# Optimization experiments

Measured on AMD Instinct MI355X. Metric: run time of the kernel, lower is better.

Reference implementation:

```python
import jax, jax.numpy as jnp
import numpy as np

B, INPUT_DIM, N = 8, 1, 4096
DIM, DEPTH, HEADS, DIM_HEAD = 512, 4, 8, 64
WINDOW = 128
NUM_CLASSES = 10
INNER = int(DIM * 4 * 2 / 3)  # 1365 (GEGLU FeedForward inner dim)
LN_EPS = 1e-5


def setup_inputs() -> dict:
    key = jax.random.key(0)
    ks = jax.random.split(key, 12)
    s = 0.02
    inner_qkv = HEADS * DIM_HEAD
    return {
        "x": jax.random.normal(ks[0], (B, INPUT_DIM, N), dtype=jnp.float32),
        "lin_emb_w": jax.random.normal(ks[1], (DIM, INPUT_DIM), dtype=jnp.float32) * s,
        "lin_emb_b": jnp.zeros((DIM,), dtype=jnp.float32),
        "qkv_w": jax.random.normal(ks[2], (DEPTH, 3 * inner_qkv, DIM), dtype=jnp.float32) * s,
        "out_w": jax.random.normal(ks[3], (DEPTH, DIM, inner_qkv), dtype=jnp.float32) * s,
        "ff_ln_g": jnp.ones((DEPTH, DIM), dtype=jnp.float32),
        "ff_ln_b": jnp.zeros((DEPTH, DIM), dtype=jnp.float32),
        "ff_w1": jax.random.normal(ks[4], (DEPTH, 2 * INNER, DIM), dtype=jnp.float32) * s,
        "ff_w2": jax.random.normal(ks[5], (DEPTH, DIM, INNER), dtype=jnp.float32) * s,
        "proj_w": jax.random.normal(ks[6], (NUM_CLASSES, DIM), dtype=jnp.float32) * s,
        "proj_b": jnp.zeros((NUM_CLASSES,), dtype=jnp.float32),
    }


def _layer_norm(x, g, b):
    mu = jnp.mean(x, axis=-1, keepdims=True)
    var = jnp.mean(jnp.square(x - mu), axis=-1, keepdims=True)
    return (x - mu) * jax.lax.rsqrt(var + LN_EPS) * g + b


def _local_attention(q, k, v, w):
    # q,k,v: (b, h, n, d). Non-causal sliding window: each window of size w
    # attends to windows [i-1, i, i+1] (look_backward=1, look_forward=1),
    # with out-of-range key positions masked (lucidrains LocalAttention,
    # autopad=True, exact_windowsize=False). n is a multiple of w here.
    b, h, n, d = q.shape
    nw = n // w
    scale = d ** -0.5
    qw = q.reshape(b, h, nw, w, d) * scale
    kw = k.reshape(b, h, nw, w, d)
    vw = v.reshape(b, h, nw, w, d)

    def look_around(t):  # (b,h,nw,w,d) -> (b,h,nw,3w,d)
        tp = jnp.pad(t, ((0, 0), (0, 0), (1, 1), (0, 0), (0, 0)))
        return jnp.concatenate([tp[:, :, i:i + nw] for i in range(3)], axis=3)

    k3 = look_around(kw)
    v3 = look_around(vw)

    # validity mask for boundary windows (fake keys from padding)
    win = jnp.arange(nw)
    kpos = (win[:, None] - 1) * w + jnp.arange(3 * w)[None, :]  # (nw, 3w)
    valid = (kpos >= 0) & (kpos < n)

    scores = jnp.einsum('bhnqd,bhnkd->bhnqk', qw, k3)  # (b,h,nw,w,3w)
    scores = jnp.where(valid[None, None, :, None, :], scores,
                       jnp.finfo(scores.dtype).min)
    attn = jax.nn.softmax(scores, axis=-1)
    out = jnp.einsum('bhnqk,bhnkd->bhnqd', attn, v3)
    return out.reshape(b, h, n, d)


def reference(x, lin_emb_w, lin_emb_b, qkv_w, out_w, ff_ln_g, ff_ln_b,
              ff_w1, ff_w2, proj_w, proj_b):
    b = x.shape[0]
    h = jnp.einsum('bdn,ed->bne', x, lin_emb_w) + lin_emb_b  # (b, n, dim)
    for l in range(DEPTH):
        # --- LocalMHA (no prenorm) + residual ---
        qkv = jnp.einsum('bnd,ed->bne', h, qkv_w[l])
        q, k, v = jnp.split(qkv, 3, axis=-1)
        def heads(t):
            return t.reshape(b, N, HEADS, DIM_HEAD).transpose(0, 2, 1, 3)
        o = _local_attention(heads(q), heads(k), heads(v), WINDOW)
        o = o.transpose(0, 2, 1, 3).reshape(b, N, HEADS * DIM_HEAD)
        h = jnp.einsum('bne,de->bnd', o, out_w[l]) + h
        # --- GEGLU FeedForward (prenorm inside) + residual ---
        y = _layer_norm(h, ff_ln_g[l], ff_ln_b[l])
        y = jnp.einsum('bnd,ed->bne', y, ff_w1[l])
        u, gate = jnp.split(y, 2, axis=-1)
        y = u * jax.nn.gelu(gate, approximate=False)
        h = h + jnp.einsum('bne,de->bnd', y, ff_w2[l])
    pooled = h.mean(axis=1)  # mean_pooling
    return pooled @ proj_w.T + proj_b
```

## Files before the change

### kernel.cpp

```cpp
#include <hip/hip_runtime.h>
#include <hip/hip_bf16.h>
#include <math.h>

typedef __attribute__((ext_vector_type(8))) short short8;
typedef __attribute__((ext_vector_type(4))) float f32x4;

__device__ __forceinline__ short f2bf(float f){
  unsigned u = __float_as_uint(f);
  u = (u + 0x7FFFu + ((u >> 16) & 1u)) >> 16;
  return (short)u;
}

__global__ void cast_bf16_kernel(const float* __restrict__ s, short* __restrict__ d, int n){
  int i = blockIdx.x * 256 + threadIdx.x;
  if (i < n) d[i] = f2bf(s[i]);
}

__global__ void w1p_kernel(const float* __restrict__ s, short* __restrict__ d){
  int i = blockIdx.x * 256 + threadIdx.x;
  int c  = i & 511;
  int rl = i >> 9;
  int r  = rl % 2816;
  int l  = rl / 2816;
  float v = 0.f;
  if (r < 2730){
    int sr = (r & 1) ? (1365 + (r >> 1)) : (r >> 1);
    v = s[((size_t)l * 2730 + sr) * 512 + c];
  }
  d[i] = f2bf(v);
}

__global__ void w2p_kernel(const float* __restrict__ s, short* __restrict__ d){
  int i = blockIdx.x * 256 + threadIdx.x;
  int c = i % 1408;
  int r = i / 1408;
  float v = (c < 1365) ? s[(size_t)r * 1365 + c] : 0.f;
  d[i] = f2bf(v);
}

__global__ void embed_kernel(const float* __restrict__ x, const float* __restrict__ w,
                             const float* __restrict__ bias, float* __restrict__ hf,
                             short* __restrict__ hb){
  long i = (long)blockIdx.x * 256 + threadIdx.x;
  long row = i >> 9; int e = (int)(i & 511);
  float v = x[row] * w[e] + bias[e];
  hf[i] = v;
  hb[i] = f2bf(v);
}

template<int EPI>
__global__ __launch_bounds__(256, 2)
void gemm_bt(const short* __restrict__ A, const short* __restrict__ B, int K,
             float* __restrict__ Cres, short* __restrict__ Cbf, int ldcb)
{
  __shared__ short As[128 * 64];
  __shared__ short Bs[128 * 64];
  const int tid  = threadIdx.x;
  const int lane = tid & 63;
  const int w    = tid >> 6;
  const int wr   = (w >> 1) * 64, wc = (w & 1) * 64;
  const long tm = (long)blockIdx.y * 128, tn = (long)blockIdx.x * 128;

  f32x4 acc[4][4];
  #pragma unroll
  for (int i = 0; i < 4; i++)
    #pragma unroll
    for (int j = 0; j < 4; j++)
      acc[i][j] = (f32x4){0.f, 0.f, 0.f, 0.f};

  const int row_s = tid >> 3;
  const int c_s   = tid & 7;

  for (int k0 = 0; k0 < K; k0 += 64){
    __syncthreads();
    #pragma unroll
    for (int r = 0; r < 4; r++){
      int row = row_s + r * 32;
      short8 av = *(const short8*)(A + (tm + row) * K + k0 + c_s * 8);
      short8 bv = *(const short8*)(B + (tn + row) * K + k0 + c_s * 8);
      int off = (row * 128 + c_s * 16) ^ ((row & 7) << 4);
      *(short8*)((char*)As + off) = av;
      *(short8*)((char*)Bs + off) = bv;
    }
    __syncthreads();
    #pragma unroll
    for (int kk = 0; kk < 2; kk++){
      short8 a[4], b[4];
      int ac = (kk * 32 + (lane >> 4) * 8) * 2;
      #pragma unroll
      for (int i = 0; i < 4; i++){
        int ar = wr + i * 16 + (lane & 15);
        a[i] = *(const short8*)((char*)As + ((ar * 128 + ac) ^ ((ar & 7) << 4)));
        int br = wc + i * 16 + (lane & 15);
        b[i] = *(const short8*)((char*)Bs + ((br * 128 + ac) ^ ((br & 7) << 4)));
      }
      #pragma unroll
      for (int i = 0; i < 4; i++)
        #pragma unroll
        for (int j = 0; j < 4; j++)
          acc[i][j] = __builtin_amdgcn_mfma_f32_16x16x32_bf16(a[i], b[j], acc[i][j], 0, 0, 0);
    }
  }

  #pragma unroll
  for (int i = 0; i < 4; i++){
    #pragma unroll
    for (int j = 0; j < 4; j++){
      #pragma unroll
      for (int v = 0; v < 4; v++){
        long row = tm + wr + i * 16 + (lane >> 4) * 4 + v;
        long col = tn + wc + j * 16 + (lane & 15);
        float x = acc[i][j][v];
        if (EPI == 0){
          Cbf[row * ldcb + col] = f2bf(x);
        } else if (EPI == 1){
          float rr = x + Cres[row * 512 + col];
          Cres[row * 512 + col] = rr;
        } else if (EPI == 2){
          float rr = x + Cres[row * 512 + col];
          Cres[row * 512 + col] = rr;
          Cbf[row * 512 + col] = f2bf(rr);
        } else {
          float other = __shfl_xor(x, 1);
          if ((lane & 1) == 0){
            float gate = other;
            float gg = 0.5f * gate * (1.f + erff(gate * 0.70710678118f));
            Cbf[row * ldcb + (col >> 1)] = f2bf(x * gg);
          }
        }
      }
    }
  }
}

__global__ __launch_bounds__(256, 2)
void attn_kernel(const short* __restrict__ qkv, short* __restrict__ o)
{
  __shared__ short Ks[128 * 64];
  __shared__ short Vt[64 * 136];
  __shared__ short Ps[4 * 32 * 128];
  const int win = blockIdx.x, hh = blockIdx.y, b = blockIdx.z;
  const int tid = threadIdx.x, lane = tid & 63, w = tid >> 6;
  const long qrow0 = (long)b * 4096 + (long)win * 128;

  short8 qf[2][2];
  #pragma unroll
  for (int i = 0; i < 2; i++)
    #pragma unroll
    for (int kk = 0; kk < 2; kk++)
      qf[i][kk] = *(const short8*)(qkv + (qrow0 + w * 32 + i * 16 + (lane & 15)) * 1536
                                   + hh * 64 + kk * 32 + (lane >> 4) * 8);

  f32x4 oacc[2][4];
  #pragma unroll
  for (int i = 0; i < 2; i++)
    #pragma unroll
    for (int j = 0; j < 4; j++)
      oacc[i][j] = (f32x4){0.f, 0.f, 0.f, 0.f};
  float rs[2][4];
  #pragma unroll
  for (int i = 0; i < 2; i++)
    #pragma unroll
    for (int v = 0; v < 4; v++)
      rs[i][v] = 0.f;

  const int row_s = tid >> 3, c_s = tid & 7;
  for (int cc = 0; cc < 3; cc++){
    int kw = win - 1 + cc;
    if (kw < 0 || kw >= 32) continue;
    const long krow0 = (long)b * 4096 + (long)kw * 128;
    __syncthreads();
    #pragma unroll
    for (int r = 0; r < 4; r++){
      int row = row_s + r * 32;
      const short* src = qkv + (krow0 + row) * 1536 + hh * 64;
      short8 kv = *(const short8*)(src + 512 + c_s * 8);
      *(short8*)((char*)Ks + ((row * 128 + c_s * 16) ^ ((row & 7) << 4))) = kv;
      short8 vv = *(const short8*)(src + 1024 + c_s * 8);
      #pragma unroll
      for (int e = 0; e < 8; e++) Vt[(c_s * 8 + e) * 136 + row] = vv[e];
    }
    __syncthreads();

    f32x4 sacc[2][8];
    #pragma unroll
    for (int i = 0; i < 2; i++)
      #pragma unroll
      for (int j = 0; j < 8; j++)
        sacc[i][j] = (f32x4){0.f, 0.f, 0.f, 0.f};
    #pragma unroll
    for (int kk = 0; kk < 2; kk++){
      short8 bb[8];
      int ac = (kk * 32 + (lane >> 4) * 8) * 2;
      #pragma unroll
      for (int j = 0; j < 8; j++){
        int br = j * 16 + (lane & 15);
        bb[j] = *(const short8*)((char*)Ks + ((br * 128 + ac) ^ ((br & 7) << 4)));
      }
      #pragma unroll
      for (int i = 0; i < 2; i++)
        #pragma unroll
        for (int j = 0; j < 8; j++)
          sacc[i][j] = __builtin_amdgcn_mfma_f32_16x16x32_bf16(qf[i][kk], bb[j], sacc[i][j], 0, 0, 0);
    }

    short* myPs = Ps + w * 32 * 128;
    float psum[2][4];
    #pragma unroll
    for (int i = 0; i < 2; i++)
      #pragma unroll
      for (int v = 0; v < 4; v++)
        psum[i][v] = 0.f;
    #pragma unroll
    for (int i = 0; i < 2; i++)
      #pragma unroll
      for (int j = 0; j < 8; j++)
        #pragma unroll
        for (int v = 0; v < 4; v++){
          float p = expf(0.125f * sacc[i][j][v]);
          psum[i][v] += p;
          int prow = i * 16 + (lane >> 4) * 4 + v;
          int pcb  = (j * 16 + (lane & 15)) * 2;
          *(short*)((char*)myPs + ((prow * 256 + pcb) ^ ((prow & 7) << 4))) = f2bf(p);
        }
    #pragma unroll
    for (int i = 0; i < 2; i++)
      #pragma unroll
      for (int v = 0; v < 4; v++){
        float s = psum[i][v];
        s += __shfl_xor(s, 1); s += __shfl_xor(s, 2);
        s += __shfl_xor(s, 4); s += __shfl_xor(s, 8);
        rs[i][v] += s;
      }
    __syncthreads();

    #pragma unroll
    for (int kk = 0; kk < 4; kk++){
      short8 pa[2], vb[4];
      int kb = (kk * 32 + (lane >> 4) * 8) * 2;
      #pragma unroll
      for (int i = 0; i < 2; i++){
        int pr = i * 16 + (lane & 15);
        pa[i] = *(const short8*)((char*)myPs + ((pr * 256 + kb) ^ ((pr & 7) << 4)));
      }
      #pragma unroll
      for (int j = 0; j < 4; j++){
        int vr = j * 16 + (lane & 15);
        vb[j] = *(const short8*)((char*)Vt + (vr * 272 + kb));
      }
      #pragma unroll
      for (int i = 0; i < 2; i++)
        #pragma unroll
        for (int j = 0; j < 4; j++)
          oacc[i][j] = __builtin_amdgcn_mfma_f32_16x16x32_bf16(pa[i], vb[j], oacc[i][j], 0, 0, 0);
    }
  }

  #pragma unroll
  for (int i = 0; i < 2; i++)
    #pragma unroll
    for (int j = 0; j < 4; j++)
      #pragma unroll
      for (int v = 0; v < 4; v++){
        long row = qrow0 + w * 32 + i * 16 + (lane >> 4) * 4 + v;
        int col = hh * 64 + j * 16 + (lane & 15);
        o[row * 512 + col] = f2bf(oacc[i][j][v] / rs[i][v]);
      }
}

__global__ __launch_bounds__(256)
void ln_kernel(const float* __restrict__ h, const float* __restrict__ g,
               const float* __restrict__ be, short* __restrict__ y)
{
  long row = (long)blockIdx.x * 4 + (threadIdx.x >> 6);
  int lane = threadIdx.x & 63;
  const float* x = h + row * 512 + lane * 8;
  float4 a0 = *(const float4*)x;
  float4 a1 = *(const float4*)(x + 4);
  float v[8] = {a0.x, a0.y, a0.z, a0.w, a1.x, a1.y, a1.z, a1.w};
  float s = 0.f, sq = 0.f;
  #pragma unroll
  for (int j = 0; j < 8; j++){ s += v[j]; sq += v[j] * v[j]; }
  #pragma unroll
  for (int m = 1; m <= 32; m <<= 1){ s += __shfl_xor(s, m); sq += __shfl_xor(sq, m); }
  float mu = s * (1.f / 512.f);
  float var = sq * (1.f / 512.f) - mu * mu;
  float rstd = rsqrtf(var + 1e-5f);
  short* yo = y + row * 512 + lane * 8;
  #pragma unroll
  for (int j = 0; j < 8; j++){
    int c = lane * 8 + j;
    yo[j] = f2bf((v[j] - mu) * rstd * g[c] + be[c]);
  }
}

__global__ void pool_partial(const float* __restrict__ h, float* __restrict__ part){
  int b = blockIdx.x, ch = blockIdx.y, t = threadIdx.x;
  float s0 = 0.f, s1 = 0.f;
  const float* base = h + ((long)b * 4096 + ch * 128) * 512;
  for (int n = 0; n < 128; n++){
    s0 += base[(long)n * 512 + t];
    s1 += base[(long)n * 512 + t + 256];
  }
  part[((b * 32 + ch) * 512) + t] = s0;
  part[((b * 32 + ch) * 512) + t + 256] = s1;
}

__global__ void pool_proj(const float* __restrict__ part, const float* __restrict__ pw,
                          const float* __restrict__ pb, float* __restrict__ out){
  __shared__ float pooled[512];
  __shared__ float red[4];
  int b = blockIdx.x, t = threadIdx.x;
  int lane = t & 63, w = t >> 6;
  float s0 = 0.f, s1 = 0.f;
  for (int ch = 0; ch < 32; ch++){
    s0 += part[((b * 32 + ch) * 512) + t];
    s1 += part[((b * 32 + ch) * 512) + t + 256];
  }
  pooled[t] = s0 * (1.f / 4096.f);
  pooled[t + 256] = s1 * (1.f / 4096.f);
  __syncthreads();
  for (int cls = 0; cls < 10; cls++){
    float p = pooled[t] * pw[cls * 512 + t] + pooled[t + 256] * pw[cls * 512 + t + 256];
    p += __shfl_xor(p, 1); p += __shfl_xor(p, 2); p += __shfl_xor(p, 4);
    p += __shfl_xor(p, 8); p += __shfl_xor(p, 16); p += __shfl_xor(p, 32);
    if (lane == 0) red[w] = p;
    __syncthreads();
    if (t == 0) out[b * 10 + cls] = red[0] + red[1] + red[2] + red[3] + pb[cls];
    __syncthreads();
  }
}

extern "C" void kernel_launch(void* const* d_in, const int* in_sizes, int n_in,
                              void* d_out, int out_size, void* d_ws, size_t ws_size,
                              hipStream_t stream)
{
  const float* x      = (const float*)d_in[0];
  const float* lin_w  = (const float*)d_in[1];
  const float* lin_b  = (const float*)d_in[2];
  const float* qkvw_f = (const float*)d_in[3];
  const float* outw_f = (const float*)d_in[4];
  const float* lng    = (const float*)d_in[5];
  const float* lnb    = (const float*)d_in[6];
  const float* w1_f   = (const float*)d_in[7];
  const float* w2_f   = (const float*)d_in[8];
  const float* projw  = (const float*)d_in[9];
  const float* projb  = (const float*)d_in[10];
  float* out = (float*)d_out;

  char* ws = (char*)d_ws;
  float* hf32 = (float*)(ws);
  short* abuf = (short*)(ws + 67108864);
  short* qkvb = (short*)(ws + 100663296);
  short* gbuf = qkvb;
  short* obuf = (short*)(ws + 201326592);
  float* part = (float*)(ws + 234881024);
  short* wqkv = (short*)(ws + 235405312);
  short* wout = (short*)(ws + 247988224);
  short* w1p  = (short*)(ws + 250085376);
  short* w2p  = (short*)(ws + 261619712);

  cast_bf16_kernel<<<12288, 256, 0, stream>>>(qkvw_f, wqkv, 4 * 1536 * 512);
  cast_bf16_kernel<<<4096, 256, 0, stream>>>(outw_f, wout, 4 * 512 * 512);
  w1p_kernel<<<22528, 256, 0, stream>>>(w1_f, w1p);
  w2p_kernel<<<11264, 256, 0, stream>>>(w2_f, w2p);
  embed_kernel<<<65536, 256, 0, stream>>>(x, lin_w, lin_b, hf32, abuf);

  for (int l = 0; l < 4; l++){
    gemm_bt<0><<<dim3(12, 256), 256, 0, stream>>>(abuf, wqkv + (size_t)l * 1536 * 512, 512,
                                                  nullptr, qkvb, 1536);
    attn_kernel<<<dim3(32, 8, 8), 256, 0, stream>>>(qkvb, obuf);
    gemm_bt<1><<<dim3(4, 256), 256, 0, stream>>>(obuf, wout + (size_t)l * 512 * 512, 512,
                                                 hf32, nullptr, 0);
    ln_kernel<<<8192, 256, 0, stream>>>(hf32, lng + l * 512, lnb + l * 512, abuf);
    gemm_bt<3><<<dim3(22, 256), 256, 0, stream>>>(abuf, w1p + (size_t)l * 2816 * 512, 512,
                                                  nullptr, gbuf, 1408);
    gemm_bt<2><<<dim3(4, 256), 256, 0, stream>>>(gbuf, w2p + (size_t)l * 512 * 1408, 1408,
                                                 hf32, abuf, 512);
  }
  pool_partial<<<dim3(8, 32), 256, 0, stream>>>(hf32, part);
  pool_proj<<<8, 256, 0, stream>>>(part, projw, projb, out);
}
```

Measured before the change: 1.916 ms.

## Replace 128x128 GEMM with pipelined 256x256 direct-to-LDS double-buffered GEMM

Replaces the 128x128 tiled GEMM with a 256x256-tile, 512-thread kernel. It uses global_load_lds direct copies into a double-buffered shared memory ring, interleaves prefetch with MFMA phases under explicit barriers and setprio, and adds XCD-aware block swizzling. The GEGLU weight layout is regrouped in blocks of 16 so u and gate land in adjacent accumulator tiles, which removes the cross-lane shuffle. erff is replaced by a polynomial approximation. The risks are tail quantization with fewer, larger tiles, a heavy LDS footprint of 128KB that limits occupancy, and the approximation error of the polynomial GELU.

```diff
diff --git a/kernel.cpp b/kernel.cpp
--- a/kernel.cpp
+++ b/kernel.cpp
@@ -4,11 +4,22 @@
 
 typedef __attribute__((ext_vector_type(8))) short short8;
 typedef __attribute__((ext_vector_type(4))) float f32x4;
+
+#define MFMA16 __builtin_amdgcn_mfma_f32_16x16x32_bf16
 
 __device__ __forceinline__ short f2bf(float f){
   unsigned u = __float_as_uint(f);
   u = (u + 0x7FFFu + ((u >> 16) & 1u)) >> 16;
   return (short)u;
+}
+
+__device__ __forceinline__ float gelu_phi(float g){
+  float ax = fabsf(g) * 0.70710678118f;
+  float t  = 1.f / (1.f + 0.3275911f * ax);
+  float pp = ((((1.061405429f * t - 1.453152027f) * t + 1.421413741f) * t
+               - 0.284496736f) * t + 0.254829592f) * t;
+  float e  = 1.f - pp * __expf(-ax * ax);
+  return 0.5f + copysignf(0.5f, g) * e;
 }
 
 __global__ void cast_bf16_kernel(const float* __restrict__ s, short* __restrict__ d, int n){
@@ -22,9 +33,11 @@
   int rl = i >> 9;
   int r  = rl % 2816;
   int l  = rl / 2816;
+  int g  = r >> 5, sfx = r & 31;
+  int j  = g * 16 + (sfx & 15);
   float v = 0.f;
-  if (r < 2730){
-    int sr = (r & 1) ? (1365 + (r >> 1)) : (r >> 1);
+  if (j < 1365){
+    int sr = (sfx < 16) ? j : 1365 + j;
     v = s[((size_t)l * 2730 + sr) * 512 + c];
   }
   d[i] = f2bf(v);
@@ -49,83 +62,171 @@
 }
 
 template<int EPI>
-__global__ __launch_bounds__(256, 2)
-void gemm_bt(const short* __restrict__ A, const short* __restrict__ B, int K,
+__global__ __launch_bounds__(512, 2)
+void gemm256(const short* __restrict__ A, const short* __restrict__ B, int K,
              float* __restrict__ Cres, short* __restrict__ Cbf, int ldcb)
 {
-  __shared__ short As[128 * 64];
-  __shared__ short Bs[128 * 64];
+  __shared__ short As[2][256][64];
+  __shared__ short Bs[2][256][64];
+  char* smA = (char*)As;
+  char* smB = (char*)Bs;
+
   const int tid  = threadIdx.x;
   const int lane = tid & 63;
   const int w    = tid >> 6;
-  const int wr   = (w >> 1) * 64, wc = (w & 1) * 64;
-  const long tm = (long)blockIdx.y * 128, tn = (long)blockIdx.x * 128;
-
-  f32x4 acc[4][4];
-  #pragma unroll
-  for (int i = 0; i < 4; i++)
+  const int wm   = w >> 2;
+  const int wn   = w & 3;
+  const int NT   = K >> 6;
+
+  const int nwg = gridDim.x * gridDim.y;
+  const int f   = blockIdx.y * gridDim.x + blockIdx.x;
+  const int sw  = (f & 7) * (nwg >> 3) + (f >> 3);
+  const long tm = (long)(sw / gridDim.x) * 256;
+  const long tn = (long)(sw % gridDim.x) * 256;
+
+  const int r0 = tid >> 3;
+  const int c0 = (tid & 7) ^ (r0 & 7);
+  const short* aS = A + (tm + r0) * (long)K + c0 * 8;
+  const short* bS = B + (tn + r0) * (long)K + c0 * 8;
+  const int ldsW0 = w * 1024;
+  const int ldsW1 = 8192 + w * 1024;
+  const long halfA = 128 * (long)K;
+
+  auto stgA = [&](int dstoff, const short* srcp){
+    __builtin_amdgcn_global_load_lds((const __attribute__((address_space(1))) void*)(srcp),
+        (__attribute__((address_space(3))) void*)(smA + dstoff + ldsW0), 16, 0, 0);
+    __builtin_amdgcn_global_load_lds((const __attribute__((address_space(1))) void*)(srcp + 64 * (long)K),
+        (__attribute__((address_space(3))) void*)(smA + dstoff + ldsW1), 16, 0, 0);
+  };
+  auto stgB = [&](int dstoff, const short* srcp){
+    __builtin_amdgcn_global_load_lds((const __attribute__((address_space(1))) void*)(srcp),
+        (__attribute__((address_space(3))) void*)(smB + dstoff + ldsW0), 16, 0, 0);
+    __builtin_amdgcn_global_load_lds((const __attribute__((address_space(1))) void*)(srcp + 64 * (long)K),
+        (__attribute__((address_space(3))) void*)(smB + dstoff + ldsW1), 16, 0, 0);
+  };
+
+  f32x4 acc[8][4];
+  #pragma unroll
+  for (int i = 0; i < 8; i++)
     #pragma unroll
     for (int j = 0; j < 4; j++)
       acc[i][j] = (f32x4){0.f, 0.f, 0.f, 0.f};
 
-  const int row_s = tid >> 3;
-  const int c_s   = tid & 7;
-
-  for (int k0 = 0; k0 < K; k0 += 64){
-    __syncthreads();
-    #pragma unroll
-    for (int r = 0; r < 4; r++){
-      int row = row_s + r * 32;
-      short8 av = *(const short8*)(A + (tm + row) * K + k0 + c_s * 8);
-      short8 bv = *(const short8*)(B + (tn + row) * K + k0 + c_s * 8);
-      int off = (row * 128 + c_s * 16) ^ ((row & 7) << 4);
-      *(short8*)((char*)As + off) = av;
-      *(short8*)((char*)Bs + off) = bv;
-    }
-    __syncthreads();
-    #pragma unroll
-    for (int kk = 0; kk < 2; kk++){
-      short8 a[4], b[4];
-      int ac = (kk * 32 + (lane >> 4) * 8) * 2;
-      #pragma unroll
-      for (int i = 0; i < 4; i++){
-        int ar = wr + i * 16 + (lane & 15);
-        a[i] = *(const short8*)((char*)As + ((ar * 128 + ac) ^ ((ar & 7) << 4)));
-        int br = wc + i * 16 + (lane & 15);
-        b[i] = *(const short8*)((char*)Bs + ((br * 128 + ac) ^ ((br & 7) << 4)));
-      }
-      #pragma unroll
-      for (int i = 0; i < 4; i++)
+  const int rb  = (lane & 15) * 128;
+  const int ct0 = (((lane >> 4)    ) ^ (lane & 7)) * 16;
+  const int ct1 = ((4 + (lane >> 4)) ^ (lane & 7)) * 16;
+
+  stgB(0,             bS);
+  stgA(0,             aS);
+  stgA(16384,         aS + halfA);
+  stgB(16384,         bS + halfA);
+  if (NT > 1){
+    stgB(32768,         bS + 64);
+    stgA(32768,         aS + 64);
+    stgA(32768 + 16384, aS + halfA + 64);
+  }
+  asm volatile("s_waitcnt vmcnt(6)" ::: "memory");
+  __builtin_amdgcn_s_barrier();
+
+  for (int t = 0; t < NT; ++t){
+    const int cur = (t & 1) * 32768;
+    const int nxt = 32768 - cur;
+    const bool s1 = (t + 1 < NT), s2 = (t + 2 < NT);
+    const long o1 = (long)(t + 1) * 64, o2 = (long)(t + 2) * 64;
+    short8 a0[8], a1[8], bb[4][2];
+
+    #pragma unroll
+    for (int ni = 0; ni < 4; ni++){
+      bb[ni][0] = *(const short8*)(smB + cur + wn * 8192 + ni * 2048 + rb + ct0);
+      bb[ni][1] = *(const short8*)(smB + cur + wn * 8192 + ni * 2048 + rb + ct1);
+    }
+    #pragma unroll
+    for (int mi = 0; mi < 8; mi++)
+      a0[mi] = *(const short8*)(smA + cur + wm * 16384 + mi * 2048 + rb + ct0);
+    if (s1) stgB(nxt + 16384, bS + halfA + o1);
+    asm volatile("s_waitcnt lgkmcnt(0)" ::: "memory");
+    __builtin_amdgcn_sched_barrier(0);
+    __builtin_amdgcn_s_barrier();
+    __builtin_amdgcn_s_setprio(1);
+    #pragma unroll
+    for (int mi = 0; mi < 8; mi++){
+      acc[mi][0] = MFMA16(a0[mi], bb[0][0], acc[mi][0], 0, 0, 0);
+      acc[mi][1] = MFMA16(a0[mi], bb[1][0], acc[mi][1], 0, 0, 0);
+    }
+    __builtin_amdgcn_s_setprio(0);
+    __builtin_amdgcn_s_barrier();
+
+    #pragma unroll
+    for (int mi = 0; mi < 8; mi++)
+      a1[mi] = *(const short8*)(smA + cur + wm * 16384 + mi * 2048 + rb + ct1);
+    if (s2) stgB(cur, bS + o2);
+    asm volatile("s_waitcnt lgkmcnt(0)" ::: "memory");
+    __builtin_amdgcn_sched_barrier(0);
+    __builtin_amdgcn_s_barrier();
+    __builtin_amdgcn_s_setprio(1);
+    #pragma unroll
+    for (int mi = 0; mi < 8; mi++){
+      acc[mi][2] = MFMA16(a0[mi], bb[2][0], acc[mi][2], 0, 0, 0);
+      acc[mi][3] = MFMA16(a0[mi], bb[3][0], acc[mi][3], 0, 0, 0);
+    }
+    __builtin_amdgcn_s_setprio(0);
+    __builtin_amdgcn_s_barrier();
+
+    if (s2) stgA(cur, aS + o2);
+    __builtin_amdgcn_s_barrier();
+    __builtin_amdgcn_s_setprio(1);
+    #pragma unroll
+    for (int mi = 0; mi < 8; mi++){
+      acc[mi][0] = MFMA16(a1[mi], bb[0][1], acc[mi][0], 0, 0, 0);
+      acc[mi][1] = MFMA16(a1[mi], bb[1][1], acc[mi][1], 0, 0, 0);
+    }
+    __builtin_amdgcn_s_setprio(0);
+    __builtin_amdgcn_s_barrier();
+
+    if (s2) stgA(cur + 16384, aS + halfA + o2);
+    if (t < NT - 2) asm volatile("s_waitcnt vmcnt(6)" ::: "memory");
+    else            asm volatile("s_waitcnt vmcnt(0)" ::: "memory");
+    __builtin_amdgcn_s_barrier();
+    __builtin_amdgcn_s_setprio(1);
+    #pragma unroll
+    for (int mi = 0; mi < 8; mi++){
+      acc[mi][2] = MFMA16(a1[mi], bb[2][1], acc[mi][2], 0, 0, 0);
+      acc[mi][3] = MFMA16(a1[mi], bb[3][1], acc[mi][3], 0, 0, 0);
+    }
+    __builtin_amdgcn_s_setprio(0);
+    __builtin_amdgcn_s_barrier();
+  }
+
+  #pragma unroll
+  for (int mi = 0; mi < 8; mi++){
+    if (EPI == 3){
+      #pragma unroll
+      for (int p = 0; p < 2; p++){
         #pragma unroll
-        for (int j = 0; j < 4; j++)
-          acc[i][j] = __builtin_amdgcn_mfma_f32_16x16x32_bf16(a[i], b[j], acc[i][j], 0, 0, 0);
-    }
-  }
-
-  #pragma unroll
-  for (int i = 0; i < 4; i++){
-    #pragma unroll
-    for (int j = 0; j < 4; j++){
-      #pragma unroll
-      for (int v = 0; v < 4; v++){
-        long row = tm + wr + i * 16 + (lane >> 4) * 4 + v;
-        long col = tn + wc + j * 16 + (lane & 15);
-        float x = acc[i][j][v];
-        if (EPI == 0){
-          Cbf[row * ldcb + col] = f2bf(x);
-        } else if (EPI == 1){
-          float rr = x + Cres[row * 512 + col];
-          Cres[row * 512 + col] = rr;
-        } else if (EPI == 2){
-          float rr = x + Cres[row * 512 + col];
-          Cres[row * 512 + col] = rr;
-          Cbf[row * 512 + col] = f2bf(rr);
-        } else {
-          float other = __shfl_xor(x, 1);
-          if ((lane & 1) == 0){
-            float gate = other;
-            float gg = 0.5f * gate * (1.f + erff(gate * 0.70710678118f));
-            Cbf[row * ldcb + (col >> 1)] = f2bf(x * gg);
+        for (int v = 0; v < 4; v++){
+          long row = tm + wm * 128 + mi * 16 + (lane >> 4) * 4 + v;
+          long col = (tn >> 1) + wn * 32 + p * 16 + (lane & 15);
+          float u = acc[mi][2 * p][v];
+          float g = acc[mi][2 * p + 1][v];
+          Cbf[row * ldcb + col] = f2bf(u * g * gelu_phi(g));
+        }
+      }
+    } else {
+      #pragma unroll
+      for (int ni = 0; ni < 4; ni++){
+        #pragma unroll
+        for (int v = 0; v < 4; v++){
+          long row = tm + wm * 128 + mi * 16 + (lane >> 4) * 4 + v;
+          long col = tn + wn * 64 + ni * 16 + (lane & 15);
+          float x = acc[mi][ni][v];
+          if (EPI == 0){
+            Cbf[row * ldcb + col] = f2bf(x);
+          } else if (EPI == 1){
+            Cres[row * 512 + col] = x + Cres[row * 512 + col];
+          } else {
+            float rr = x + Cres[row * 512 + col];
+            Cres[row * 512 + col] = rr;
+            Cbf[row * 512 + col] = f2bf(rr);
           }
         }
       }
@@ -190,18 +291,18 @@
         sacc[i][j] = (f32x4){0.f, 0.f, 0.f, 0.f};
     #pragma unroll
     for (int kk = 0; kk < 2; kk++){
-      short8 bb[8];
+      short8 bbk[8];
       int ac = (kk * 32 + (lane >> 4) * 8) * 2;
       #pragma unroll
       for (int j = 0; j < 8; j++){
         int br = j * 16 + (lane & 15);
-        bb[j] = *(const short8*)((char*)Ks + ((br * 128 + ac) ^ ((br & 7) << 4)));
+        bbk[j] = *(const short8*)((char*)Ks + ((br * 128 + ac) ^ ((br & 7) << 4)));
       }
       #pragma unroll
       for (int i = 0; i < 2; i++)
         #pragma unroll
         for (int j = 0; j < 8; j++)
-          sacc[i][j] = __builtin_amdgcn_mfma_f32_16x16x32_bf16(qf[i][kk], bb[j], sacc[i][j], 0, 0, 0);
+          sacc[i][j] = MFMA16(qf[i][kk], bbk[j], sacc[i][j], 0, 0, 0);
     }
 
     short* myPs = Ps + w * 32 * 128;
@@ -252,7 +353,7 @@
       for (int i = 0; i < 2; i++)
         #pragma unroll
         for (int j = 0; j < 4; j++)
-          oacc[i][j] = __builtin_amdgcn_mfma_f32_16x16x32_bf16(pa[i], vb[j], oacc[i][j], 0, 0, 0);
+          oacc[i][j] = MFMA16(pa[i], vb[j], oacc[i][j], 0, 0, 0);
     }
   }
 
@@ -367,15 +468,15 @@
   embed_kernel<<<65536, 256, 0, stream>>>(x, lin_w, lin_b, hf32, abuf);
 
   for (int l = 0; l < 4; l++){
-    gemm_bt<0><<<dim3(12, 256), 256, 0, stream>>>(abuf, wqkv + (size_t)l * 1536 * 512, 512,
-                                                  nullptr, qkvb, 1536);
+    gemm256<0><<<dim3(6, 128), 512, 0, stream>>>(abuf, wqkv + (size_t)l * 1536 * 512, 512,
+                                                 nullptr, qkvb, 1536);
     attn_kernel<<<dim3(32, 8, 8), 256, 0, stream>>>(qkvb, obuf);
-    gemm_bt<1><<<dim3(4, 256), 256, 0, stream>>>(obuf, wout + (size_t)l * 512 * 512, 512,
+    gemm256<1><<<dim3(2, 128), 512, 0, stream>>>(obuf, wout + (size_t)l * 512 * 512, 512,
                                                  hf32, nullptr, 0);
     ln_kernel<<<8192, 256, 0, stream>>>(hf32, lng + l * 512, lnb + l * 512, abuf);
-    gemm_bt<3><<<dim3(22, 256), 256, 0, stream>>>(abuf, w1p + (size_t)l * 2816 * 512, 512,
+    gemm256<3><<<dim3(11, 128), 512, 0, stream>>>(abuf, w1p + (size_t)l * 2816 * 512, 512,
                                                   nullptr, gbuf, 1408);
-    gemm_bt<2><<<dim3(4, 256), 256, 0, stream>>>(gbuf, w2p + (size_t)l * 512 * 1408, 1408,
+    gemm256<2><<<dim3(2, 128), 512, 0, stream>>>(gbuf, w2p + (size_t)l * 512 * 1408, 1408,
                                                  hf32, abuf, 512);
   }
   pool_partial<<<dim3(8, 32), 256, 0, stream>>>(hf32, part);
```

Result: faster. 1.823 ms (-4.9%).
